# Kernel optimization log

Measured on AMD Instinct MI355X. Metric: run time of the kernel, lower is better.

The kernel has to match this reference:

```python
import jax, jax.numpy as jnp
import numpy as np

MAX_DISP = 4  # max_displacement == pad_size; kernel_size == 1, stride == 1


def setup_inputs() -> dict:
    key = jax.random.key(0)
    k1, k2 = jax.random.split(key)
    B, C, H, W = 8, 256, 96, 128
    in1 = jax.random.normal(k1, (B, C, H, W), dtype=jnp.float32)
    in2 = jax.random.normal(k2, (B, C, H, W), dtype=jnp.float32)
    return {"in1": in1, "in2": in2}


def reference(in1, in2):
    # Local cost-volume correlation: for each pixel (h,w) and each displacement
    # (dy,dx) in [-4,4]^2, mean over channels of in1[...,h,w] * in2[...,h+dy,w+dx]
    # with zero padding outside the image. Output: [B, 81, H, W].
    B, C, H, W = in1.shape
    d = MAX_DISP
    p2 = jnp.pad(in2, ((0, 0), (0, 0), (d, d), (d, d)))
    outs = []
    # fixed 9x9 displacement set (structural, not a data-dim loop)
    for dy in range(2 * d + 1):
        for dx in range(2 * d + 1):
            shifted = jax.lax.dynamic_slice(p2, (0, 0, dy, dx), (B, C, H, W))
            outs.append(jnp.mean(in1 * shifted, axis=1))  # [B, H, W]
    return jnp.stack(outs, axis=1)  # [B, 81, H, W]
```

## Files before the change

### kernel.cpp

```cpp
#include <hip/hip_runtime.h>


#define CH 256
#define HH 96
#define WW 128
#define CS (HH * WW)

__device__ __forceinline__ float wshr1(float x) {
  union { float f; int i; } u, o;
  u.f = x;
  o.i = __builtin_amdgcn_update_dpp(0, u.i, 0x138, 0xF, 0xF, true);
  return o.f;
}
__device__ __forceinline__ float wshl1(float x) {
  union { float f; int i; } u, o;
  u.f = x;
  o.i = __builtin_amdgcn_update_dpp(0, u.i, 0x130, 0xF, 0xF, true);
  return o.f;
}

__global__ __launch_bounds__(256, 4) void corr_dpp(
    const float* __restrict__ in1, const float* __restrict__ in2,
    float* __restrict__ out)
{
  const int j    = blockIdx.x;
  const int xcd  = j & 7;
  const int s    = j >> 3;
  const int dy   = s % 9;
  const int tq   = s / 9;
  const int tile = tq * 8 + xcd;
  const int band = tile % 12;
  const int b    = tile / 12;
  const int dyo  = dy - 4;

  const int tid  = threadIdx.x;
  const int wv   = tid >> 6;
  const int lane = tid & 63;
  const int r    = lane >> 5;
  const int g    = lane & 31;
  const int h    = band * 8 + wv * 2 + r;
  const int px   = g << 2;
  const int r2   = h + dyo;
  const bool rowok = (unsigned)r2 < (unsigned)HH;
  const int r2c  = r2 < 0 ? 0 : (r2 > HH - 1 ? HH - 1 : r2);

  const float* p1 = in1 + ((size_t)b * CH * HH + h)   * WW + px;
  const float* p2 = in2 + ((size_t)b * CH * HH + r2c) * WW + px;

  float acc[4][9];
#pragma unroll
  for (int p = 0; p < 4; ++p)
#pragma unroll
    for (int d = 0; d < 9; ++d) acc[p][d] = 0.f;

#pragma unroll 2
  for (int c = 0; c < CH; ++c) {
    float4 a4 = *(const float4*)p1;  p1 += CS;
    float4 m4 = *(const float4*)p2;  p2 += CS;

    float w[12];
    w[0] = wshr1(m4.x); w[1] = wshr1(m4.y); w[2] = wshr1(m4.z); w[3] = wshr1(m4.w);
    w[4] = m4.x; w[5] = m4.y; w[6] = m4.z; w[7] = m4.w;
    w[8] = wshl1(m4.x); w[9] = wshl1(m4.y); w[10] = wshl1(m4.z); w[11] = wshl1(m4.w);

    const float av[4] = {a4.x, a4.y, a4.z, a4.w};
#pragma unroll
    for (int p = 0; p < 4; ++p)
#pragma unroll
      for (int d = 0; d < 9; ++d)
        acc[p][d] = fmaf(av[p], w[p + d], acc[p][d]);
  }

  const float sc = 1.0f / (float)CH;
  float* po = out + (((size_t)b * 81 + dy * 9) * HH + h) * WW + px;
#pragma unroll
  for (int d = 0; d < 9; ++d) {
    float v[4];
#pragma unroll
    for (int p = 0; p < 4; ++p) {
      const int col2 = px + p + d - 4;
      const bool ok  = rowok && ((unsigned)col2 < (unsigned)WW);
      v[p] = ok ? acc[p][d] * sc : 0.f;
    }
    *(float4*)po = make_float4(v[0], v[1], v[2], v[3]);
    po += (size_t)CS;
  }
}

extern "C" void kernel_launch(void* const* d_in, const int* in_sizes, int n_in,
                              void* d_out, int out_size, void* d_ws, size_t ws_size,
                              hipStream_t stream) {
  const float* in1 = (const float*)d_in[0];
  const float* in2 = (const float*)d_in[1];
  float* out = (float*)d_out;
  hipLaunchKernelGGL(corr_dpp, dim3(864), dim3(256), 0, stream, in1, in2, out);
}
```

Before: 334.8 us.

## Split channel reduction across two thread halves with LDS combine

```diff
diff --git a/kernel.cpp b/kernel.cpp
--- a/kernel.cpp
+++ b/kernel.cpp
@@ -2,6 +2,7 @@
 
 
 #define CH 256
+#define HALFC 128
 #define HH 96
 #define WW 128
 #define CS (HH * WW)
@@ -19,7 +20,7 @@
   return o.f;
 }
 
-__global__ __launch_bounds__(256, 4) void corr_dpp(
+__global__ __launch_bounds__(512, 4) void corr_split(
     const float* __restrict__ in1, const float* __restrict__ in2,
     float* __restrict__ out)
 {
@@ -34,8 +35,10 @@
   const int dyo  = dy - 4;
 
   const int tid  = threadIdx.x;
-  const int wv   = tid >> 6;
-  const int lane = tid & 63;
+  const int half = tid >> 8;
+  const int t    = tid & 255;
+  const int wv   = t >> 6;
+  const int lane = t & 63;
   const int r    = lane >> 5;
   const int g    = lane & 31;
   const int h    = band * 8 + wv * 2 + r;
@@ -44,8 +47,10 @@
   const bool rowok = (unsigned)r2 < (unsigned)HH;
   const int r2c  = r2 < 0 ? 0 : (r2 > HH - 1 ? HH - 1 : r2);
 
-  const float* p1 = in1 + ((size_t)b * CH * HH + h)   * WW + px;
-  const float* p2 = in2 + ((size_t)b * CH * HH + r2c) * WW + px;
+  const float* __restrict__ p1 =
+      in1 + (((size_t)b * CH + half * HALFC) * HH + h)   * WW + px;
+  const float* __restrict__ p2 =
+      in2 + (((size_t)b * CH + half * HALFC) * HH + r2c) * WW + px;
 
   float acc[4][9];
 #pragma unroll
@@ -54,7 +59,7 @@
     for (int d = 0; d < 9; ++d) acc[p][d] = 0.f;
 
 #pragma unroll 2
-  for (int c = 0; c < CH; ++c) {
+  for (int c = 0; c < HALFC; ++c) {
     float4 a4 = *(const float4*)p1;  p1 += CS;
     float4 m4 = *(const float4*)p2;  p2 += CS;
 
@@ -71,19 +76,35 @@
         acc[p][d] = fmaf(av[p], w[p + d], acc[p][d]);
   }
 
-  const float sc = 1.0f / (float)CH;
-  float* po = out + (((size_t)b * 81 + dy * 9) * HH + h) * WW + px;
+  __shared__ float red[256][37];
+  if (half) {
 #pragma unroll
-  for (int d = 0; d < 9; ++d) {
-    float v[4];
+    for (int p = 0; p < 4; ++p)
 #pragma unroll
-    for (int p = 0; p < 4; ++p) {
-      const int col2 = px + p + d - 4;
-      const bool ok  = rowok && ((unsigned)col2 < (unsigned)WW);
-      v[p] = ok ? acc[p][d] * sc : 0.f;
+      for (int d = 0; d < 9; ++d) red[t][p * 9 + d] = acc[p][d];
+  }
+  __syncthreads();
+
+  if (!half) {
+#pragma unroll
+    for (int p = 0; p < 4; ++p)
+#pragma unroll
+      for (int d = 0; d < 9; ++d) acc[p][d] += red[t][p * 9 + d];
+
+    const float sc = 1.0f / (float)CH;
+    float* po = out + (((size_t)b * 81 + dy * 9) * HH + h) * WW + px;
+#pragma unroll
+    for (int d = 0; d < 9; ++d) {
+      float v[4];
+#pragma unroll
+      for (int p = 0; p < 4; ++p) {
+        const int col2 = px + p + d - 4;
+        const bool ok  = rowok && ((unsigned)col2 < (unsigned)WW);
+        v[p] = ok ? acc[p][d] * sc : 0.f;
+      }
+      *(float4*)po = make_float4(v[0], v[1], v[2], v[3]);
+      po += (size_t)CS;
     }
-    *(float4*)po = make_float4(v[0], v[1], v[2], v[3]);
-    po += (size_t)CS;
   }
 }
 
@@ -93,5 +114,5 @@
   const float* in1 = (const float*)d_in[0];
   const float* in2 = (const float*)d_in[1];
   float* out = (float*)d_out;
-  hipLaunchKernelGGL(corr_dpp, dim3(864), dim3(256), 0, stream, in1, in2, out);
+  hipLaunchKernelGGL(corr_split, dim3(864), dim3(512), 0, stream, in1, in2, out);
 }
```

New measurement: 302.1 us. 9.8% less time.

## Use two pixels per thread with full-wave row mapping to raise thread parallelism

Applied to the files above, without the earlier changes.

```diff
diff --git a/kernel.cpp b/kernel.cpp
--- a/kernel.cpp
+++ b/kernel.cpp
@@ -19,7 +19,7 @@
   return o.f;
 }
 
-__global__ __launch_bounds__(256, 4) void corr_dpp(
+__global__ __launch_bounds__(256, 6) void corr_tlp(
     const float* __restrict__ in1, const float* __restrict__ in2,
     float* __restrict__ out)
 {
@@ -29,60 +29,57 @@
   const int dy   = s % 9;
   const int tq   = s / 9;
   const int tile = tq * 8 + xcd;
-  const int band = tile % 12;
-  const int b    = tile / 12;
+  const int band = tile % 24;
+  const int b    = tile / 24;
   const int dyo  = dy - 4;
 
   const int tid  = threadIdx.x;
   const int wv   = tid >> 6;
   const int lane = tid & 63;
-  const int r    = lane >> 5;
-  const int g    = lane & 31;
-  const int h    = band * 8 + wv * 2 + r;
-  const int px   = g << 2;
+  const int h    = band * 4 + wv;
+  const int px   = lane << 1;
   const int r2   = h + dyo;
   const bool rowok = (unsigned)r2 < (unsigned)HH;
   const int r2c  = r2 < 0 ? 0 : (r2 > HH - 1 ? HH - 1 : r2);
 
-  const float* p1 = in1 + ((size_t)b * CH * HH + h)   * WW + px;
-  const float* p2 = in2 + ((size_t)b * CH * HH + r2c) * WW + px;
+  const float* __restrict__ p1 = in1 + ((size_t)b * CH * HH + h)   * WW + px;
+  const float* __restrict__ p2 = in2 + ((size_t)b * CH * HH + r2c) * WW + px;
 
-  float acc[4][9];
+  float acc[2][9];
 #pragma unroll
-  for (int p = 0; p < 4; ++p)
+  for (int p = 0; p < 2; ++p)
 #pragma unroll
     for (int d = 0; d < 9; ++d) acc[p][d] = 0.f;
 
 #pragma unroll 2
   for (int c = 0; c < CH; ++c) {
-    float4 a4 = *(const float4*)p1;  p1 += CS;
-    float4 m4 = *(const float4*)p2;  p2 += CS;
+    const float2 a = *(const float2*)p1;  p1 += CS;
+    const float2 m = *(const float2*)p2;  p2 += CS;
 
-    float w[12];
-    w[0] = wshr1(m4.x); w[1] = wshr1(m4.y); w[2] = wshr1(m4.z); w[3] = wshr1(m4.w);
-    w[4] = m4.x; w[5] = m4.y; w[6] = m4.z; w[7] = m4.w;
-    w[8] = wshl1(m4.x); w[9] = wshl1(m4.y); w[10] = wshl1(m4.z); w[11] = wshl1(m4.w);
+    float w[10];
+    w[2] = wshr1(m.x);  w[3] = wshr1(m.y);
+    w[0] = wshr1(w[2]); w[1] = wshr1(w[3]);
+    w[4] = m.x;         w[5] = m.y;
+    w[6] = wshl1(m.x);  w[7] = wshl1(m.y);
+    w[8] = wshl1(w[6]); w[9] = wshl1(w[7]);
 
-    const float av[4] = {a4.x, a4.y, a4.z, a4.w};
 #pragma unroll
-    for (int p = 0; p < 4; ++p)
-#pragma unroll
-      for (int d = 0; d < 9; ++d)
-        acc[p][d] = fmaf(av[p], w[p + d], acc[p][d]);
+    for (int d = 0; d < 9; ++d) {
+      acc[0][d] = fmaf(a.x, w[d],     acc[0][d]);
+      acc[1][d] = fmaf(a.y, w[d + 1], acc[1][d]);
+    }
   }
 
   const float sc = 1.0f / (float)CH;
   float* po = out + (((size_t)b * 81 + dy * 9) * HH + h) * WW + px;
 #pragma unroll
   for (int d = 0; d < 9; ++d) {
-    float v[4];
-#pragma unroll
-    for (int p = 0; p < 4; ++p) {
-      const int col2 = px + p + d - 4;
-      const bool ok  = rowok && ((unsigned)col2 < (unsigned)WW);
-      v[p] = ok ? acc[p][d] * sc : 0.f;
-    }
-    *(float4*)po = make_float4(v[0], v[1], v[2], v[3]);
+    float2 v;
+    const int c0 = px + d - 4;
+    const int c1 = px + 1 + d - 4;
+    v.x = (rowok && (unsigned)c0 < (unsigned)WW) ? acc[0][d] * sc : 0.f;
+    v.y = (rowok && (unsigned)c1 < (unsigned)WW) ? acc[1][d] * sc : 0.f;
+    *(float2*)po = v;
     po += (size_t)CS;
   }
 }
@@ -93,5 +90,5 @@
   const float* in1 = (const float*)d_in[0];
   const float* in2 = (const float*)d_in[1];
   float* out = (float*)d_out;
-  hipLaunchKernelGGL(corr_dpp, dim3(864), dim3(256), 0, stream, in1, in2, out);
+  hipLaunchKernelGGL(corr_tlp, dim3(1728), dim3(256), 0, stream, in1, in2, out);
 }
```

New measurement: 351.5 us. 1.05x slower.

## Stage shared input rows in LDS across all nine dy offsets per block

Applied to the files above, without the earlier changes.

```diff
diff --git a/kernel.cpp b/kernel.cpp
--- a/kernel.cpp
+++ b/kernel.cpp
@@ -5,6 +5,11 @@
 #define HH 96
 #define WW 128
 #define CS (HH * WW)
+#define KC 8
+#define NCHUNK (CH / KC)
+#define SLOTS 12
+#define LDW 132
+#define PIECES (KC * SLOTS * 32)
 
 __device__ __forceinline__ float wshr1(float x) {
   union { float f; int i; } u, o;
@@ -19,68 +24,117 @@
   return o.f;
 }
 
-__global__ __launch_bounds__(256, 4) void corr_dpp(
+__global__ __launch_bounds__(576, 4) void corr_lds(
     const float* __restrict__ in1, const float* __restrict__ in2,
     float* __restrict__ out)
 {
   const int j    = blockIdx.x;
-  const int xcd  = j & 7;
-  const int s    = j >> 3;
-  const int dy   = s % 9;
-  const int tq   = s / 9;
-  const int tile = tq * 8 + xcd;
-  const int band = tile % 12;
-  const int b    = tile / 12;
-  const int dyo  = dy - 4;
+  const int b    = j & 7;
+  const int band = j >> 3;
+  const int h0   = band * 2;
 
-  const int tid  = threadIdx.x;
-  const int wv   = tid >> 6;
-  const int lane = tid & 63;
-  const int r    = lane >> 5;
-  const int g    = lane & 31;
-  const int h    = band * 8 + wv * 2 + r;
-  const int px   = g << 2;
-  const int r2   = h + dyo;
-  const bool rowok = (unsigned)r2 < (unsigned)HH;
-  const int r2c  = r2 < 0 ? 0 : (r2 > HH - 1 ? HH - 1 : r2);
+  const int tid = threadIdx.x;
+  const int dy  = tid >> 6;
+  const int r   = (tid >> 5) & 1;
+  const int pxg = tid & 31;
+  const int px0 = pxg << 2;
+  const int h   = h0 + r;
 
-  const float* p1 = in1 + ((size_t)b * CH * HH + h)   * WW + px;
-  const float* p2 = in2 + ((size_t)b * CH * HH + r2c) * WW + px;
+  __shared__ float lds[KC][SLOTS][LDW];
+  float* const lp = &lds[0][0][0];
 
-  float acc[4][9];
+  const float* gp[6];
+  int lw[6];
+  bool val[6];
 #pragma unroll
-  for (int p = 0; p < 4; ++p)
+  for (int k = 0; k < 6; ++k) {
+    const int f = tid + 576 * k;
+    val[k] = (f < PIECES);
+    const int fc = val[k] ? f : 0;
+    const int c   = fc / (SLOTS * 32);
+    const int rem = fc - c * (SLOTS * 32);
+    const int sl  = rem >> 5;
+    const int pg  = rem & 31;
+    lw[k] = (c * SLOTS + sl) * LDW + pg * 4;
+    int row;
+    const float* basep;
+    if (sl < 2) { row = h0 + sl; basep = in1; }
+    else {
+      row = h0 - 6 + sl;
+      row = row < 0 ? 0 : (row > HH - 1 ? HH - 1 : row);
+      basep = in2;
+    }
+    gp[k] = basep + ((size_t)(b * CH + c) * HH + row) * WW + pg * 4;
+  }
+
+  float acc[9][4];
 #pragma unroll
-    for (int d = 0; d < 9; ++d) acc[p][d] = 0.f;
+  for (int d = 0; d < 9; ++d)
+#pragma unroll
+    for (int p = 0; p < 4; ++p) acc[d][p] = 0.f;
 
-#pragma unroll 2
-  for (int c = 0; c < CH; ++c) {
-    float4 a4 = *(const float4*)p1;  p1 += CS;
-    float4 m4 = *(const float4*)p2;  p2 += CS;
+  float4 L0, L1, L2, L3, L4, L5;
+  if (val[0]) L0 = *(const float4*)gp[0];
+  if (val[1]) L1 = *(const float4*)gp[1];
+  if (val[2]) L2 = *(const float4*)gp[2];
+  if (val[3]) L3 = *(const float4*)gp[3];
+  if (val[4]) L4 = *(const float4*)gp[4];
+  if (val[5]) L5 = *(const float4*)gp[5];
 
-    float w[12];
-    w[0] = wshr1(m4.x); w[1] = wshr1(m4.y); w[2] = wshr1(m4.z); w[3] = wshr1(m4.w);
-    w[4] = m4.x; w[5] = m4.y; w[6] = m4.z; w[7] = m4.w;
-    w[8] = wshl1(m4.x); w[9] = wshl1(m4.y); w[10] = wshl1(m4.z); w[11] = wshl1(m4.w);
+  const int in1off = r * LDW + px0;
+  const int in2off = (2 + r + dy) * LDW + px0;
 
-    const float av[4] = {a4.x, a4.y, a4.z, a4.w};
+#pragma unroll 1
+  for (int chunk = 0; ; ++chunk) {
+    if (val[0]) *(float4*)(lp + lw[0]) = L0;
+    if (val[1]) *(float4*)(lp + lw[1]) = L1;
+    if (val[2]) *(float4*)(lp + lw[2]) = L2;
+    if (val[3]) *(float4*)(lp + lw[3]) = L3;
+    if (val[4]) *(float4*)(lp + lw[4]) = L4;
+    if (val[5]) *(float4*)(lp + lw[5]) = L5;
+    __syncthreads();
+
+    if (chunk < NCHUNK - 1) {
+      if (val[0]) { gp[0] += (size_t)KC * CS; L0 = *(const float4*)gp[0]; }
+      if (val[1]) { gp[1] += (size_t)KC * CS; L1 = *(const float4*)gp[1]; }
+      if (val[2]) { gp[2] += (size_t)KC * CS; L2 = *(const float4*)gp[2]; }
+      if (val[3]) { gp[3] += (size_t)KC * CS; L3 = *(const float4*)gp[3]; }
+      if (val[4]) { gp[4] += (size_t)KC * CS; L4 = *(const float4*)gp[4]; }
+      if (val[5]) { gp[5] += (size_t)KC * CS; L5 = *(const float4*)gp[5]; }
+    }
+
 #pragma unroll
-    for (int p = 0; p < 4; ++p)
+    for (int cc = 0; cc < KC; ++cc) {
+      const float4 a4 = *(const float4*)(lp + cc * (SLOTS * LDW) + in1off);
+      const float4 m  = *(const float4*)(lp + cc * (SLOTS * LDW) + in2off);
+
+      float w[12];
+      w[0] = wshr1(m.x); w[1] = wshr1(m.y); w[2] = wshr1(m.z); w[3] = wshr1(m.w);
+      w[4] = m.x; w[5] = m.y; w[6] = m.z; w[7] = m.w;
+      w[8] = wshl1(m.x); w[9] = wshl1(m.y); w[10] = wshl1(m.z); w[11] = wshl1(m.w);
+
+      const float av[4] = {a4.x, a4.y, a4.z, a4.w};
 #pragma unroll
       for (int d = 0; d < 9; ++d)
-        acc[p][d] = fmaf(av[p], w[p + d], acc[p][d]);
+#pragma unroll
+        for (int p = 0; p < 4; ++p)
+          acc[d][p] = fmaf(av[p], w[p + d], acc[d][p]);
+    }
+
+    if (chunk == NCHUNK - 1) break;
+    __syncthreads();
   }
 
   const float sc = 1.0f / (float)CH;
-  float* po = out + (((size_t)b * 81 + dy * 9) * HH + h) * WW + px;
+  const bool rowok = (unsigned)(h + dy - 4) < (unsigned)HH;
+  float* po = out + (((size_t)b * 81 + dy * 9) * HH + h) * WW + px0;
 #pragma unroll
   for (int d = 0; d < 9; ++d) {
     float v[4];
 #pragma unroll
     for (int p = 0; p < 4; ++p) {
-      const int col2 = px + p + d - 4;
-      const bool ok  = rowok && ((unsigned)col2 < (unsigned)WW);
-      v[p] = ok ? acc[p][d] * sc : 0.f;
+      const int col2 = px0 + p + d - 4;
+      v[p] = (rowok && (unsigned)col2 < (unsigned)WW) ? acc[d][p] * sc : 0.f;
     }
     *(float4*)po = make_float4(v[0], v[1], v[2], v[3]);
     po += (size_t)CS;
@@ -93,5 +147,5 @@
   const float* in1 = (const float*)d_in[0];
   const float* in2 = (const float*)d_in[1];
   float* out = (float*)d_out;
-  hipLaunchKernelGGL(corr_dpp, dim3(864), dim3(256), 0, stream, in1, in2, out);
+  hipLaunchKernelGGL(corr_lds, dim3(384), dim3(576), 0, stream, in1, in2, out);
 }
```

Result: slower. 587.4 us (+75.4%).
